# Optimization experiments

Hardware: AMD Instinct MI355X
Metric: run time of the kernel (lower is better)

Reference implementation:

```python
import jax, jax.numpy as jnp
import numpy as np

NUM_HEADS = 16
LN_EPS = 1e-5


def _layernorm(x, g, b):
    mu = jnp.mean(x, axis=-1, keepdims=True)
    var = jnp.mean(jnp.square(x - mu), axis=-1, keepdims=True)
    return (x - mu) * jax.lax.rsqrt(var + LN_EPS) * g + b


def setup_inputs() -> dict:
    key = jax.random.key(0)
    ks = jax.random.split(key, 8)
    B, S, D = 4, 2048, 1024
    s = 0.02  # small init so softmax/layernorm stay well-conditioned
    return {
        "x": jax.random.normal(ks[0], (B, S, D), jnp.float32),
        "wq_w": jax.random.normal(ks[1], (D, D), jnp.float32) * s,
        "wq_b": jnp.zeros((D,), jnp.float32),
        "wk_w": jax.random.normal(ks[2], (D, D), jnp.float32) * s,
        "wk_b": jnp.zeros((D,), jnp.float32),
        "wv_w": jax.random.normal(ks[3], (D, D), jnp.float32) * s,
        "wv_b": jnp.zeros((D,), jnp.float32),
        "ln1_g": jnp.ones((D,), jnp.float32),
        "ln1_b": jnp.zeros((D,), jnp.float32),
        "lin1_w": jax.random.normal(ks[4], (D, D), jnp.float32) * s,
        "lin1_b": jnp.zeros((D,), jnp.float32),
        "ln2_g": jnp.ones((D,), jnp.float32),
        "ln2_b": jnp.zeros((D,), jnp.float32),
    }


def reference(x, wq_w, wq_b, wk_w, wk_b, wv_w, wv_b,
              ln1_g, ln1_b, lin1_w, lin1_b, ln2_g, ln2_b):
    B, S, D = x.shape
    H = NUM_HEADS
    dh = D // H

    def proj(w, b):
        # torch Linear: x @ w.T + b ; split heads -> [B,H,S,dh]
        return (x @ w.T + b).reshape(B, S, H, dh).transpose(0, 2, 1, 3)

    q, k, v = proj(wq_w, wq_b), proj(wk_w, wk_b), proj(wv_w, wv_b)

    scores = jnp.einsum("bhqd,bhkd->bhqk", q, k) / jnp.sqrt(jnp.float32(dh))
    causal = jnp.tril(jnp.ones((S, S), jnp.bool_))  # True = attend
    scores = jnp.where(causal[None, None], scores, -jnp.inf)
    probs = jax.nn.softmax(scores, axis=-1)
    attn = jnp.einsum("bhqk,bhkd->bhqd", probs, v)
    attn = attn.transpose(0, 2, 1, 3).reshape(B, S, D)

    h = _layernorm(x + attn, ln1_g, ln1_b)
    h = _layernorm(h + (h @ lin1_w.T + lin1_b), ln2_g, ln2_b)
    return h
```

## Files before the change

kernel.cpp:

```cpp
#include <hip/hip_runtime.h>
#include <math.h>

#define B_  4
#define S_  2048
#define D_  1024
#define H_  16
#define DH_ 64
#define M_  (B_*S_)

typedef unsigned short ushort_t;
typedef __attribute__((ext_vector_type(8))) __bf16 bf16x8;
typedef __attribute__((ext_vector_type(4))) float f32x4;
typedef __attribute__((ext_vector_type(8))) unsigned short us8;
typedef __attribute__((ext_vector_type(4))) unsigned short us4;

__device__ __forceinline__ ushort_t f2bf(float f) {
    unsigned int u = __float_as_uint(f);
    u = (u + 0x7fffu + ((u >> 16) & 1u)) >> 16;
    return (ushort_t)u;
}

#define GLD16(gp, lp) __builtin_amdgcn_global_load_lds( \
    (const __attribute__((address_space(1))) void*)(gp), \
    (__attribute__((address_space(3))) void*)(lp), 16, 0, 0)

#define WAIT_VM0()   __builtin_amdgcn_s_waitcnt(0x0F70)
#define WAIT_VM4()   __builtin_amdgcn_s_waitcnt(0x0F74)
#define MEMFENCE()   asm volatile("" ::: "memory")

__global__ __launch_bounds__(256)
void cvt_kernel(const float* __restrict__ src, ushort_t* __restrict__ dst, int n)
{
    int i = (blockIdx.x * 256 + threadIdx.x) * 8;
    if (i >= n) return;
    float4 a = *(const float4*)(src + i);
    float4 b = *(const float4*)(src + i + 4);
    us8 r;
    r[0] = f2bf(a.x); r[1] = f2bf(a.y); r[2] = f2bf(a.z); r[3] = f2bf(a.w);
    r[4] = f2bf(b.x); r[5] = f2bf(b.y); r[6] = f2bf(b.z); r[7] = f2bf(b.w);
    *(us8*)(dst + i) = r;
}

__global__ __launch_bounds__(256)
void cvt_w4(const float* __restrict__ w0, const float* __restrict__ w1,
            const float* __restrict__ w2, const float* __restrict__ w3,
            ushort_t* __restrict__ dst)
{
    const int ten = blockIdx.y;
    const float* s = (ten == 0) ? w0 : (ten == 1) ? w1 : (ten == 2) ? w2 : w3;
    ushort_t* d = dst + (size_t)ten * (D_ * D_);
    int i = (blockIdx.x * 256 + threadIdx.x) * 8;
    float4 a = *(const float4*)(s + i);
    float4 b = *(const float4*)(s + i + 4);
    us8 r;
    r[0] = f2bf(a.x); r[1] = f2bf(a.y); r[2] = f2bf(a.z); r[3] = f2bf(a.w);
    r[4] = f2bf(b.x); r[5] = f2bf(b.y); r[6] = f2bf(b.z); r[7] = f2bf(b.w);
    *(us8*)(d + i) = r;
}

__global__ __launch_bounds__(256)
void gemm_mfma(const ushort_t* __restrict__ A, const ushort_t* __restrict__ Bw,
               const float* __restrict__ bias0, const float* __restrict__ bias1,
               const float* __restrict__ bias2,
               float* __restrict__ Yf, ushort_t* __restrict__ Qo,
               ushort_t* __restrict__ Ko, ushort_t* __restrict__ Vo,
               int K, int mode)
{
    __shared__ __align__(16) ushort_t As[128 * 32];
    __shared__ __align__(16) ushort_t Bs[128 * 32];
    const int t = threadIdx.x;
    const int lane = t & 63, wave = t >> 6;
    const int wm = wave >> 1, wn = wave & 1;
    const int m0 = blockIdx.x * 128, n0 = blockIdx.y * 128;
    const int quad = lane >> 4, l15 = lane & 15;

    const int ch0 = wave * 2, ch1 = wave * 2 + 1;
    const int srow = lane >> 2;
    const int scol = (lane & 3) * 8;
    const ushort_t* Ap0 = A  + (size_t)(m0 + ch0 * 16 + srow) * K + scol;
    const ushort_t* Ap1 = A  + (size_t)(m0 + ch1 * 16 + srow) * K + scol;
    const ushort_t* Bp0 = Bw + (size_t)(n0 + ch0 * 16 + srow) * K + scol;
    const ushort_t* Bp1 = Bw + (size_t)(n0 + ch1 * 16 + srow) * K + scol;
    ushort_t* lA0 = As + ch0 * 512;
    ushort_t* lA1 = As + ch1 * 512;
    ushort_t* lB0 = Bs + ch0 * 512;
    ushort_t* lB1 = Bs + ch1 * 512;

    f32x4 acc[4][4] = {};

    for (int k0 = 0; k0 < K; k0 += 32) {
        GLD16(Ap0 + k0, lA0);
        GLD16(Ap1 + k0, lA1);
        GLD16(Bp0 + k0, lB0);
        GLD16(Bp1 + k0, lB1);
        WAIT_VM0();
        __syncthreads();

        bf16x8 af[4], bfr[4];
        #pragma unroll
        for (int i = 0; i < 4; i++)
            af[i] = *(const bf16x8*)(As + (64 * wm + 16 * i + l15) * 32 + quad * 8);
        #pragma unroll
        for (int j = 0; j < 4; j++)
            bfr[j] = *(const bf16x8*)(Bs + (64 * wn + 16 * j + l15) * 32 + quad * 8);
        #pragma unroll
        for (int i = 0; i < 4; i++)
            #pragma unroll
            for (int j = 0; j < 4; j++)
                acc[i][j] = __builtin_amdgcn_mfma_f32_16x16x32_bf16(af[i], bfr[j], acc[i][j], 0, 0, 0);
        __syncthreads();
    }

    #pragma unroll
    for (int j = 0; j < 4; j++) {
        const int n = n0 + 64 * wn + 16 * j + l15;
        if (mode == 1) {
            const float bv = bias0[n];
            #pragma unroll
            for (int i = 0; i < 4; i++) {
                const int mrow = m0 + 64 * wm + 16 * i + quad * 4;
                float* yp = Yf + (size_t)mrow * D_ + n;
                #pragma unroll
                for (int r = 0; r < 4; r++)
                    yp[(size_t)r * D_] = acc[i][j][r] + bv;
            }
        } else {
            const int sel = n >> 10, nn = n & 1023;
            const int hh = nn >> 6, dd = nn & 63;
            const float bv = (sel == 0 ? bias0 : (sel == 1 ? bias1 : bias2))[nn];
            const float scl = (sel == 0) ? 0.125f : 1.0f;
            #pragma unroll
            for (int i = 0; i < 4; i++) {
                const int mrow = m0 + 64 * wm + 16 * i + quad * 4;
                const int b = mrow >> 11;
                const int ss = mrow & (S_ - 1);
                #pragma unroll
                for (int r = 0; r < 4; r++) {
                    const float v = (acc[i][j][r] + bv) * scl;
                    const ushort_t bvv = f2bf(v);
                    if (sel == 0)
                        Qo[(((size_t)b * H_ + hh) * S_ + ss + r) * DH_ + dd] = bvv;
                    else if (sel == 1)
                        Ko[(((size_t)b * H_ + hh) * S_ + ss + r) * DH_ + dd] = bvv;
                    else
                        Vo[(((size_t)b * H_ + hh) * DH_ + dd) * S_ + ss + r] = bvv;
                }
            }
        }
    }
}

__global__ __launch_bounds__(256, 2)
void attn_mfma(const ushort_t* __restrict__ Qb, const ushort_t* __restrict__ Kb,
               const ushort_t* __restrict__ Vt, float* __restrict__ out)
{
    __shared__ __align__(16) ushort_t Ks[2][64 * 64];
    __shared__ __align__(16) ushort_t Vs[2][64 * 64];
    __shared__ __align__(16) ushort_t Ps[8][16 * 72];
    const int t = threadIdx.x, lane = t & 63, w = t >> 6;
    const int bx = blockIdx.x;
    const int bh = blockIdx.y;
    const int quad = lane >> 4, l15 = lane & 15;
    const int rw = 32 * w;

    const int c0 = 2 * w, c1 = 2 * w + 1;
    const int srow = lane >> 3;
    const int scol = 8 * ((lane & 7) ^ srow);
    const ushort_t* KgB = Kb + (size_t)bh * S_ * DH_;
    const ushort_t* VgB = Vt + (size_t)bh * DH_ * S_;
    const ushort_t* Kg0 = KgB + (size_t)(c0 * 8 + srow) * DH_ + scol;
    const ushort_t* Kg1 = KgB + (size_t)(c1 * 8 + srow) * DH_ + scol;
    const ushort_t* Vg0 = VgB + (size_t)(c0 * 8 + srow) * S_ + scol;
    const ushort_t* Vg1 = VgB + (size_t)(c1 * 8 + srow) * S_ + scol;
    ushort_t* pw0 = Ps[w * 2 + 0];
    ushort_t* pw1 = Ps[w * 2 + 1];
    const int b = bh >> 4, hh = bh & (H_ - 1);

    for (int ph = 0; ph < 2; ph++) {
        const int qt = ph ? bx : (15 - bx);
        const int q0 = qt * 128;

        const ushort_t* qp = Qb + ((size_t)bh * S_ + q0 + rw + l15) * DH_ + quad * 8;
        const bf16x8 qf00 = *(const bf16x8*)(qp);
        const bf16x8 qf01 = *(const bf16x8*)(qp + 32);
        const bf16x8 qf10 = *(const bf16x8*)(qp + 16 * DH_);
        const bf16x8 qf11 = *(const bf16x8*)(qp + 16 * DH_ + 32);

        f32x4 o0[4] = {}, o1[4] = {};
        float m0v = -INFINITY, m1v = -INFINITY, l0v = 0.f, l1v = 0.f;

        WAIT_VM0();
        MEMFENCE();
        GLD16(Kg0, &Ks[0][c0 * 512]);
        GLD16(Kg1, &Ks[0][c1 * 512]);
        GLD16(Vg0, &Vs[0][c0 * 512]);
        GLD16(Vg1, &Vs[0][c1 * 512]);

        const int qg00 = q0 + rw;
        const int qg10 = q0 + rw + 16;
        const int last = 2 * qt + 1;

        for (int kt = 0; kt <= last; kt++) {
            const int buf = kt & 1;
            const int k0 = kt * 64;
            if (kt < last) {
                const size_t ko = (size_t)(k0 + 64) * DH_;
                GLD16(Kg0 + ko, &Ks[buf ^ 1][c0 * 512]);
                GLD16(Kg1 + ko, &Ks[buf ^ 1][c1 * 512]);
                GLD16(Vg0 + k0 + 64, &Vs[buf ^ 1][c0 * 512]);
                GLD16(Vg1 + k0 + 64, &Vs[buf ^ 1][c1 * 512]);
                WAIT_VM4();
            } else {
                WAIT_VM0();
            }
            MEMFENCE();
            __builtin_amdgcn_s_barrier();
            MEMFENCE();

            if (k0 <= qg10 + 15) {
                const bool a0 = (k0 <= qg00 + 15);
                const ushort_t* kb = Ks[buf];
                const ushort_t* vb = Vs[buf];
                const int xr = l15 & 7;

                bf16x8 kf[4][2];
                #pragma unroll
                for (int ct = 0; ct < 4; ct++)
                    #pragma unroll
                    for (int h = 0; h < 2; h++)
                        kf[ct][h] = *(const bf16x8*)(kb + (ct * 16 + l15) * 64 +
                                                     8 * ((h * 4 + quad) ^ xr));

                f32x4 sc0[4] = {}, sc1[4] = {};
                #pragma unroll
                for (int ct = 0; ct < 4; ct++) {
                    sc1[ct] = __builtin_amdgcn_mfma_f32_16x16x32_bf16(kf[ct][0], qf10, sc1[ct], 0, 0, 0);
                    sc1[ct] = __builtin_amdgcn_mfma_f32_16x16x32_bf16(kf[ct][1], qf11, sc1[ct], 0, 0, 0);
                }
                if (a0) {
                    #pragma unroll
                    for (int ct = 0; ct < 4; ct++) {
                        sc0[ct] = __builtin_amdgcn_mfma_f32_16x16x32_bf16(kf[ct][0], qf00, sc0[ct], 0, 0, 0);
                        sc0[ct] = __builtin_amdgcn_mfma_f32_16x16x32_bf16(kf[ct][1], qf01, sc0[ct], 0, 0, 0);
                    }
                }

                bf16x8 vf[4][2];
                #pragma unroll
                for (int mt = 0; mt < 4; mt++)
                    #pragma unroll
                    for (int h = 0; h < 2; h++)
                        vf[mt][h] = *(const bf16x8*)(vb + (mt * 16 + l15) * 64 +
                                                     8 * ((h * 4 + quad) ^ xr));

                if (k0 + 63 > qg10) {
                    const int qq = qg10 + l15;
                    #pragma unroll
                    for (int ct = 0; ct < 4; ct++) {
                        const int key = k0 + ct * 16 + quad * 4;
                        #pragma unroll
                        for (int r = 0; r < 4; r++)
                            if (key + r > qq) sc1[ct][r] = -INFINITY;
                    }
                }
                if (a0 && k0 + 63 > qg00) {
                    const int qq = qg00 + l15;
                    #pragma unroll
                    for (int ct = 0; ct < 4; ct++) {
                        const int key = k0 + ct * 16 + quad * 4;
                        #pragma unroll
                        for (int r = 0; r < 4; r++)
                            if (key + r > qq) sc0[ct][r] = -INFINITY;
                    }
                }

                float mx0 = -INFINITY, mx1 = sc1[0][0];
                #pragma unroll
                for (int ct = 0; ct < 4; ct++)
                    #pragma unroll
                    for (int r = 0; r < 4; r++) mx1 = fmaxf(mx1, sc1[ct][r]);
                if (a0) {
                    mx0 = sc0[0][0];
                    #pragma unroll
                    for (int ct = 0; ct < 4; ct++)
                        #pragma unroll
                        for (int r = 0; r < 4; r++) mx0 = fmaxf(mx0, sc0[ct][r]);
                }
                mx1 = fmaxf(mx1, __shfl_xor(mx1, 16));
                mx0 = fmaxf(mx0, __shfl_xor(mx0, 16));
                mx1 = fmaxf(mx1, __shfl_xor(mx1, 32));
                mx0 = fmaxf(mx0, __shfl_xor(mx0, 32));

                const float mn1 = fmaxf(m1v, mx1);
                const float al1 = __expf(m1v - mn1);
                m1v = mn1;
                const float mn0 = a0 ? fmaxf(m0v, mx0) : m0v;
                const float al0 = a0 ? __expf(m0v - mn0) : 1.f;
                m0v = mn0;

                float rs0 = 0.f, rs1 = 0.f;
                #pragma unroll
                for (int ct = 0; ct < 4; ct++) {
                    us4 pk;
                    #pragma unroll
                    for (int r = 0; r < 4; r++) {
                        const float p = __expf(sc1[ct][r] - mn1);
                        rs1 += p;
                        pk[r] = f2bf(p);
                    }
                    *(us4*)(pw1 + l15 * 72 + ct * 16 + quad * 4) = pk;
                }
                if (a0) {
                    #pragma unroll
                    for (int ct = 0; ct < 4; ct++) {
                        us4 pk;
                        #pragma unroll
                        for (int r = 0; r < 4; r++) {
                            const float p = __expf(sc0[ct][r] - mn0);
                            rs0 += p;
                            pk[r] = f2bf(p);
                        }
                        *(us4*)(pw0 + l15 * 72 + ct * 16 + quad * 4) = pk;
                    }
                }
                rs1 += __shfl_xor(rs1, 16);
                rs0 += __shfl_xor(rs0, 16);
                rs1 += __shfl_xor(rs1, 32);
                rs0 += __shfl_xor(rs0, 32);
                l1v = l1v * al1 + rs1;
                if (a0) l0v = l0v * al0 + rs0;

                #pragma unroll
                for (int mt = 0; mt < 4; mt++)
                    #pragma unroll
                    for (int r = 0; r < 4; r++) { o1[mt][r] *= al1; o0[mt][r] *= al0; }

                const bf16x8 pf10 = *(const bf16x8*)(pw1 + l15 * 72 + quad * 8);
                const bf16x8 pf11 = *(const bf16x8*)(pw1 + l15 * 72 + 32 + quad * 8);
                #pragma unroll
                for (int mt = 0; mt < 4; mt++) {
                    o1[mt] = __builtin_amdgcn_mfma_f32_16x16x32_bf16(vf[mt][0], pf10, o1[mt], 0, 0, 0);
                    o1[mt] = __builtin_amdgcn_mfma_f32_16x16x32_bf16(vf[mt][1], pf11, o1[mt], 0, 0, 0);
                }
                if (a0) {
                    const bf16x8 pf00 = *(const bf16x8*)(pw0 + l15 * 72 + quad * 8);
                    const bf16x8 pf01 = *(const bf16x8*)(pw0 + l15 * 72 + 32 + quad * 8);
                    #pragma unroll
                    for (int mt = 0; mt < 4; mt++) {
                        o0[mt] = __builtin_amdgcn_mfma_f32_16x16x32_bf16(vf[mt][0], pf00, o0[mt], 0, 0, 0);
                        o0[mt] = __builtin_amdgcn_mfma_f32_16x16x32_bf16(vf[mt][1], pf01, o0[mt], 0, 0, 0);
                    }
                }
            }
            MEMFENCE();
            __builtin_amdgcn_s_barrier();
            MEMFENCE();
        }

        {
            const float inv0 = 1.0f / l0v, inv1 = 1.0f / l1v;
            const int query0 = q0 + rw + l15;
            float* ob0 = out + ((size_t)(b * S_ + query0)) * D_ + hh * DH_ + quad * 4;
            float* ob1 = ob0 + (size_t)16 * D_;
            #pragma unroll
            for (int mt = 0; mt < 4; mt++) {
                float4 r0, r1;
                r0.x = o0[mt][0] * inv0; r0.y = o0[mt][1] * inv0;
                r0.z = o0[mt][2] * inv0; r0.w = o0[mt][3] * inv0;
                r1.x = o1[mt][0] * inv1; r1.y = o1[mt][1] * inv1;
                r1.z = o1[mt][2] * inv1; r1.w = o1[mt][3] * inv1;
                *(float4*)(ob0 + mt * 16) = r0;
                *(float4*)(ob1 + mt * 16) = r1;
            }
        }
    }
}

__global__ __launch_bounds__(256)
void add_ln_kernel(const float* __restrict__ A, const float* __restrict__ R,
                   const float* __restrict__ g, const float* __restrict__ bia,
                   float* __restrict__ out, ushort_t* __restrict__ out_bf)
{
    const int row = blockIdx.x;
    const int t   = threadIdx.x;
    const float4 av = ((const float4*)(A + (size_t)row * D_))[t];
    const float4 rv = ((const float4*)(R + (size_t)row * D_))[t];
    float4 s;
    s.x = av.x + rv.x; s.y = av.y + rv.y; s.z = av.z + rv.z; s.w = av.w + rv.w;

    float sum = s.x + s.y + s.z + s.w;
    float sq  = s.x*s.x + s.y*s.y + s.z*s.z + s.w*s.w;
    #pragma unroll
    for (int off = 32; off > 0; off >>= 1) {
        sum += __shfl_down(sum, off);
        sq  += __shfl_down(sq,  off);
    }
    __shared__ float wsum[4], wsq[4], stat[2];
    const int wid = t >> 6, lane = t & 63;
    if (lane == 0) { wsum[wid] = sum; wsq[wid] = sq; }
    __syncthreads();
    if (t == 0) {
        float S = wsum[0] + wsum[1] + wsum[2] + wsum[3];
        float Q = wsq[0]  + wsq[1]  + wsq[2]  + wsq[3];
        float mean = S * (1.0f / D_);
        float var  = Q * (1.0f / D_) - mean * mean;
        stat[0] = mean;
        stat[1] = rsqrtf(var + 1e-5f);
    }
    __syncthreads();
    const float mean = stat[0], inv = stat[1];
    const float4 gv = ((const float4*)g)[t];
    const float4 bv = ((const float4*)bia)[t];
    float4 o;
    o.x = (s.x - mean) * inv * gv.x + bv.x;
    o.y = (s.y - mean) * inv * gv.y + bv.y;
    o.z = (s.z - mean) * inv * gv.z + bv.z;
    o.w = (s.w - mean) * inv * gv.w + bv.w;
    ((float4*)(out + (size_t)row * D_))[t] = o;
    if (out_bf) {
        us4 ob;
        ob[0] = f2bf(o.x); ob[1] = f2bf(o.y); ob[2] = f2bf(o.z); ob[3] = f2bf(o.w);
        *(us4*)(out_bf + (size_t)row * D_ + t * 4) = ob;
    }
}

extern "C" void kernel_launch(void* const* d_in, const int* in_sizes, int n_in,
                              void* d_out, int out_size, void* d_ws, size_t ws_size,
                              hipStream_t stream)
{
    const float* x      = (const float*)d_in[0];
    const float* wq_w   = (const float*)d_in[1];
    const float* wq_b   = (const float*)d_in[2];
    const float* wk_w   = (const float*)d_in[3];
    const float* wk_b   = (const float*)d_in[4];
    const float* wv_w   = (const float*)d_in[5];
    const float* wv_b   = (const float*)d_in[6];
    const float* ln1_g  = (const float*)d_in[7];
    const float* ln1_b  = (const float*)d_in[8];
    const float* lin1_w = (const float*)d_in[9];
    const float* lin1_b = (const float*)d_in[10];
    const float* ln2_g  = (const float*)d_in[11];
    const float* ln2_b  = (const float*)d_in[12];
    float* out = (float*)d_out;

    char* base = (char*)d_ws;
    ushort_t* x_bf = (ushort_t*)(base);
    ushort_t* w_bf = (ushort_t*)(base + 16777216);
    ushort_t* Qbf  = (ushort_t*)(base + 25165824);
    ushort_t* Kbf  = (ushort_t*)(base + 41943040);
    ushort_t* Vtp  = (ushort_t*)(base + 58720256);
    float*    h    = (float*)   (base + 25165824);
    ushort_t* h_bf = (ushort_t*)(base + 58720256);

    cvt_kernel<<<dim3((M_ * D_) / 2048), 256, 0, stream>>>(x, x_bf, M_ * D_);
    cvt_w4<<<dim3((D_ * D_) / 2048, 4), 256, 0, stream>>>(wq_w, wk_w, wv_w, lin1_w, w_bf);

    gemm_mfma<<<dim3(M_ / 128, 3072 / 128), 256, 0, stream>>>(
        x_bf, w_bf, wq_b, wk_b, wv_b, nullptr, Qbf, Kbf, Vtp, D_, 0);

    attn_mfma<<<dim3(8, B_ * H_), 256, 0, stream>>>(Qbf, Kbf, Vtp, out);

    add_ln_kernel<<<M_, 256, 0, stream>>>(x, out, ln1_g, ln1_b, h, h_bf);

    gemm_mfma<<<dim3(M_ / 128, D_ / 128), 256, 0, stream>>>(
        h_bf, w_bf + 3 * D_ * D_, lin1_b, nullptr, nullptr, out, nullptr, nullptr, nullptr, D_, 1);

    add_ln_kernel<<<M_, 256, 0, stream>>>(h, out, ln2_g, ln2_b, out, nullptr);
}
```

Before: 345.3 us.

## Double-buffer GEMM LDS loads and pass intermediates between stages as bf16

```diff
diff --git a/kernel.cpp b/kernel.cpp
--- a/kernel.cpp
+++ b/kernel.cpp
@@ -18,6 +18,9 @@
     unsigned int u = __float_as_uint(f);
     u = (u + 0x7fffu + ((u >> 16) & 1u)) >> 16;
     return (ushort_t)u;
+}
+__device__ __forceinline__ float bf2f(ushort_t u) {
+    return __uint_as_float(((unsigned int)u) << 16);
 }
 
 #define GLD16(gp, lp) __builtin_amdgcn_global_load_lds( \
@@ -62,12 +65,12 @@
 void gemm_mfma(const ushort_t* __restrict__ A, const ushort_t* __restrict__ Bw,
                const float* __restrict__ bias0, const float* __restrict__ bias1,
                const float* __restrict__ bias2,
-               float* __restrict__ Yf, ushort_t* __restrict__ Qo,
+               ushort_t* __restrict__ Yb, ushort_t* __restrict__ Qo,
                ushort_t* __restrict__ Ko, ushort_t* __restrict__ Vo,
                int K, int mode)
 {
-    __shared__ __align__(16) ushort_t As[128 * 32];
-    __shared__ __align__(16) ushort_t Bs[128 * 32];
+    __shared__ __align__(16) ushort_t As[2][128 * 32];
+    __shared__ __align__(16) ushort_t Bs[2][128 * 32];
     const int t = threadIdx.x;
     const int lane = t & 63, wave = t >> 6;
     const int wm = wave >> 1, wn = wave & 1;
@@ -81,34 +84,47 @@
     const ushort_t* Ap1 = A  + (size_t)(m0 + ch1 * 16 + srow) * K + scol;
     const ushort_t* Bp0 = Bw + (size_t)(n0 + ch0 * 16 + srow) * K + scol;
     const ushort_t* Bp1 = Bw + (size_t)(n0 + ch1 * 16 + srow) * K + scol;
-    ushort_t* lA0 = As + ch0 * 512;
-    ushort_t* lA1 = As + ch1 * 512;
-    ushort_t* lB0 = Bs + ch0 * 512;
-    ushort_t* lB1 = Bs + ch1 * 512;
 
     f32x4 acc[4][4] = {};
 
-    for (int k0 = 0; k0 < K; k0 += 32) {
-        GLD16(Ap0 + k0, lA0);
-        GLD16(Ap1 + k0, lA1);
-        GLD16(Bp0 + k0, lB0);
-        GLD16(Bp1 + k0, lB1);
-        WAIT_VM0();
-        __syncthreads();
+    GLD16(Ap0, As[0] + ch0 * 512);
+    GLD16(Ap1, As[0] + ch1 * 512);
+    GLD16(Bp0, Bs[0] + ch0 * 512);
+    GLD16(Bp1, Bs[0] + ch1 * 512);
+
+    const int nk = K >> 5;
+    for (int ki = 0; ki < nk; ki++) {
+        const int buf = ki & 1;
+        if (ki + 1 < nk) {
+            const int k1 = (ki + 1) << 5;
+            GLD16(Ap0 + k1, As[buf ^ 1] + ch0 * 512);
+            GLD16(Ap1 + k1, As[buf ^ 1] + ch1 * 512);
+            GLD16(Bp0 + k1, Bs[buf ^ 1] + ch0 * 512);
+            GLD16(Bp1 + k1, Bs[buf ^ 1] + ch1 * 512);
+            WAIT_VM4();
+        } else {
+            WAIT_VM0();
+        }
+        MEMFENCE();
+        __builtin_amdgcn_s_barrier();
+        MEMFENCE();
 
         bf16x8 af[4], bfr[4];
         #pragma unroll
         for (int i = 0; i < 4; i++)
-            af[i] = *(const bf16x8*)(As + (64 * wm + 16 * i + l15) * 32 + quad * 8);
+            af[i] = *(const bf16x8*)(As[buf] + (64 * wm + 16 * i + l15) * 32 + quad * 8);
         #pragma unroll
         for (int j = 0; j < 4; j++)
-            bfr[j] = *(const bf16x8*)(Bs + (64 * wn + 16 * j + l15) * 32 + quad * 8);
+            bfr[j] = *(const bf16x8*)(Bs[buf] + (64 * wn + 16 * j + l15) * 32 + quad * 8);
         #pragma unroll
         for (int i = 0; i < 4; i++)
             #pragma unroll
             for (int j = 0; j < 4; j++)
                 acc[i][j] = __builtin_amdgcn_mfma_f32_16x16x32_bf16(af[i], bfr[j], acc[i][j], 0, 0, 0);
-        __syncthreads();
+
+        MEMFENCE();
+        __builtin_amdgcn_s_barrier();
+        MEMFENCE();
     }
 
     #pragma unroll
@@ -119,10 +135,10 @@
             #pragma unroll
             for (int i = 0; i < 4; i++) {
                 const int mrow = m0 + 64 * wm + 16 * i + quad * 4;
-                float* yp = Yf + (size_t)mrow * D_ + n;
+                ushort_t* yp = Yb + (size_t)mrow * D_ + n;
                 #pragma unroll
                 for (int r = 0; r < 4; r++)
-                    yp[(size_t)r * D_] = acc[i][j][r] + bv;
+                    yp[(size_t)r * D_] = f2bf(acc[i][j][r] + bv);
             }
         } else {
             const int sel = n >> 10, nn = n & 1023;
@@ -152,7 +168,7 @@
 
 __global__ __launch_bounds__(256, 2)
 void attn_mfma(const ushort_t* __restrict__ Qb, const ushort_t* __restrict__ Kb,
-               const ushort_t* __restrict__ Vt, float* __restrict__ out)
+               const ushort_t* __restrict__ Vt, ushort_t* __restrict__ outb)
 {
     __shared__ __align__(16) ushort_t Ks[2][64 * 64];
     __shared__ __align__(16) ushort_t Vs[2][64 * 64];
@@ -360,36 +376,39 @@
         {
             const float inv0 = 1.0f / l0v, inv1 = 1.0f / l1v;
             const int query0 = q0 + rw + l15;
-            float* ob0 = out + ((size_t)(b * S_ + query0)) * D_ + hh * DH_ + quad * 4;
-            float* ob1 = ob0 + (size_t)16 * D_;
+            ushort_t* ob0 = outb + ((size_t)(b * S_ + query0)) * D_ + hh * DH_ + quad * 4;
+            ushort_t* ob1 = ob0 + (size_t)16 * D_;
             #pragma unroll
             for (int mt = 0; mt < 4; mt++) {
-                float4 r0, r1;
-                r0.x = o0[mt][0] * inv0; r0.y = o0[mt][1] * inv0;
-                r0.z = o0[mt][2] * inv0; r0.w = o0[mt][3] * inv0;
-                r1.x = o1[mt][0] * inv1; r1.y = o1[mt][1] * inv1;
-                r1.z = o1[mt][2] * inv1; r1.w = o1[mt][3] * inv1;
-                *(float4*)(ob0 + mt * 16) = r0;
-                *(float4*)(ob1 + mt * 16) = r1;
+                us4 r0, r1;
+                #pragma unroll
+                for (int r = 0; r < 4; r++) {
+                    r0[r] = f2bf(o0[mt][r] * inv0);
+                    r1[r] = f2bf(o1[mt][r] * inv1);
+                }
+                *(us4*)(ob0 + mt * 16) = r0;
+                *(us4*)(ob1 + mt * 16) = r1;
             }
         }
     }
 }
 
 __global__ __launch_bounds__(256)
-void add_ln_kernel(const float* __restrict__ A, const float* __restrict__ R,
-                   const float* __restrict__ g, const float* __restrict__ bia,
-                   float* __restrict__ out, ushort_t* __restrict__ out_bf)
+void ln_f32bf(const float* __restrict__ X, const ushort_t* __restrict__ R,
+              const float* __restrict__ g, const float* __restrict__ bia,
+              ushort_t* __restrict__ out_bf)
 {
     const int row = blockIdx.x;
     const int t   = threadIdx.x;
-    const float4 av = ((const float4*)(A + (size_t)row * D_))[t];
-    const float4 rv = ((const float4*)(R + (size_t)row * D_))[t];
-    float4 s;
-    s.x = av.x + rv.x; s.y = av.y + rv.y; s.z = av.z + rv.z; s.w = av.w + rv.w;
-
-    float sum = s.x + s.y + s.z + s.w;
-    float sq  = s.x*s.x + s.y*s.y + s.z*s.z + s.w*s.w;
+    const float4 xv = ((const float4*)(X + (size_t)row * D_))[t];
+    const us4 rv = *(const us4*)(R + (size_t)row * D_ + t * 4);
+    float s0 = xv.x + bf2f(rv[0]);
+    float s1 = xv.y + bf2f(rv[1]);
+    float s2 = xv.z + bf2f(rv[2]);
+    float s3 = xv.w + bf2f(rv[3]);
+
+    float sum = s0 + s1 + s2 + s3;
+    float sq  = s0*s0 + s1*s1 + s2*s2 + s3*s3;
     #pragma unroll
     for (int off = 32; off > 0; off >>= 1) {
         sum += __shfl_down(sum, off);
@@ -411,17 +430,57 @@
     const float mean = stat[0], inv = stat[1];
     const float4 gv = ((const float4*)g)[t];
     const float4 bv = ((const float4*)bia)[t];
+    us4 ob;
+    ob[0] = f2bf((s0 - mean) * inv * gv.x + bv.x);
+    ob[1] = f2bf((s1 - mean) * inv * gv.y + bv.y);
+    ob[2] = f2bf((s2 - mean) * inv * gv.z + bv.z);
+    ob[3] = f2bf((s3 - mean) * inv * gv.w + bv.w);
+    *(us4*)(out_bf + (size_t)row * D_ + t * 4) = ob;
+}
+
+__global__ __launch_bounds__(256)
+void ln_bfbf(const ushort_t* __restrict__ Hb, const ushort_t* __restrict__ Yb,
+             const float* __restrict__ g, const float* __restrict__ bia,
+             float* __restrict__ outf)
+{
+    const int row = blockIdx.x;
+    const int t   = threadIdx.x;
+    const us4 hv = *(const us4*)(Hb + (size_t)row * D_ + t * 4);
+    const us4 yv = *(const us4*)(Yb + (size_t)row * D_ + t * 4);
+    float s0 = bf2f(hv[0]) + bf2f(yv[0]);
+    float s1 = bf2f(hv[1]) + bf2f(yv[1]);
+    float s2 = bf2f(hv[2]) + bf2f(yv[2]);
+    float s3 = bf2f(hv[3]) + bf2f(yv[3]);
+
+    float sum = s0 + s1 + s2 + s3;
+    float sq  = s0*s0 + s1*s1 + s2*s2 + s3*s3;
+    #pragma unroll
+    for (int off = 32; off > 0; off >>= 1) {
+        sum += __shfl_down(sum, off);
+        sq  += __shfl_down(sq,  off);
+    }
+    __shared__ float wsum[4], wsq[4], stat[2];
+    const int wid = t >> 6, lane = t & 63;
+    if (lane == 0) { wsum[wid] = sum; wsq[wid] = sq; }
+    __syncthreads();
+    if (t == 0) {
+        float S = wsum[0] + wsum[1] + wsum[2] + wsum[3];
+        float Q = wsq[0]  + wsq[1]  + wsq[2]  + wsq[3];
+        float mean = S * (1.0f / D_);
+        float var  = Q * (1.0f / D_) - mean * mean;
+        stat[0] = mean;
+        stat[1] = rsqrtf(var + 1e-5f);
+    }
+    __syncthreads();
+    const float mean = stat[0], inv = stat[1];
+    const float4 gv = ((const float4*)g)[t];
+    const float4 bv = ((const float4*)bia)[t];
     float4 o;
-    o.x = (s.x - mean) * inv * gv.x + bv.x;
-    o.y = (s.y - mean) * inv * gv.y + bv.y;
-    o.z = (s.z - mean) * inv * gv.z + bv.z;
-    o.w = (s.w - mean) * inv * gv.w + bv.w;
-    ((float4*)(out + (size_t)row * D_))[t] = o;
-    if (out_bf) {
-        us4 ob;
-        ob[0] = f2bf(o.x); ob[1] = f2bf(o.y); ob[2] = f2bf(o.z); ob[3] = f2bf(o.w);
-        *(us4*)(out_bf + (size_t)row * D_ + t * 4) = ob;
-    }
+    o.x = (s0 - mean) * inv * gv.x + bv.x;
+    o.y = (s1 - mean) * inv * gv.y + bv.y;
+    o.z = (s2 - mean) * inv * gv.z + bv.z;
+    o.w = (s3 - mean) * inv * gv.w + bv.w;
+    ((float4*)(outf + (size_t)row * D_))[t] = o;
 }
 
 extern "C" void kernel_launch(void* const* d_in, const int* in_sizes, int n_in,
@@ -444,13 +503,14 @@
     float* out = (float*)d_out;
 
     char* base = (char*)d_ws;
-    ushort_t* x_bf = (ushort_t*)(base);
-    ushort_t* w_bf = (ushort_t*)(base + 16777216);
-    ushort_t* Qbf  = (ushort_t*)(base + 25165824);
-    ushort_t* Kbf  = (ushort_t*)(base + 41943040);
-    ushort_t* Vtp  = (ushort_t*)(base + 58720256);
-    float*    h    = (float*)   (base + 25165824);
-    ushort_t* h_bf = (ushort_t*)(base + 58720256);
+    ushort_t* x_bf    = (ushort_t*)(base);
+    ushort_t* attn_bf = (ushort_t*)(base);
+    ushort_t* w_bf    = (ushort_t*)(base + 16777216);
+    ushort_t* Qbf     = (ushort_t*)(base + 25165824);
+    ushort_t* h_bf    = (ushort_t*)(base + 25165824);
+    ushort_t* Kbf     = (ushort_t*)(base + 41943040);
+    ushort_t* y_bf    = (ushort_t*)(base + 41943040);
+    ushort_t* Vtp     = (ushort_t*)(base + 58720256);
 
     cvt_kernel<<<dim3((M_ * D_) / 2048), 256, 0, stream>>>(x, x_bf, M_ * D_);
     cvt_w4<<<dim3((D_ * D_) / 2048, 4), 256, 0, stream>>>(wq_w, wk_w, wv_w, lin1_w, w_bf);
@@ -458,12 +518,12 @@
     gemm_mfma<<<dim3(M_ / 128, 3072 / 128), 256, 0, stream>>>(
         x_bf, w_bf, wq_b, wk_b, wv_b, nullptr, Qbf, Kbf, Vtp, D_, 0);
 
-    attn_mfma<<<dim3(8, B_ * H_), 256, 0, stream>>>(Qbf, Kbf, Vtp, out);
-
-    add_ln_kernel<<<M_, 256, 0, stream>>>(x, out, ln1_g, ln1_b, h, h_bf);
+    attn_mfma<<<dim3(8, B_ * H_), 256, 0, stream>>>(Qbf, Kbf, Vtp, attn_bf);
+
+    ln_f32bf<<<M_, 256, 0, stream>>>(x, attn_bf, ln1_g, ln1_b, h_bf);
 
     gemm_mfma<<<dim3(M_ / 128, D_ / 128), 256, 0, stream>>>(
-        h_bf, w_bf + 3 * D_ * D_, lin1_b, nullptr, nullptr, out, nullptr, nullptr, nullptr, D_, 1);
-
-    add_ln_kernel<<<M_, 256, 0, stream>>>(h, out, ln2_g, ln2_b, out, nullptr);
-}
+        h_bf, w_bf + 3 * D_ * D_, lin1_b, nullptr, nullptr, y_bf, nullptr, nullptr, nullptr, D_, 1);
+
+    ln_bfbf<<<M_, 256, 0, stream>>>(h_bf, y_bf, ln2_g, ln2_b, out);
+}
```

After: 325.8 us. -5.7%, faster.
